# Kernel tuning notes

Hardware: AMD Instinct MI355X
Metric: run time of the kernel (lower is better)

## Reference

```python
import jax, jax.numpy as jnp
import numpy as np

B, L, D = 1, 2048, 768
H, DH = 12, 64  # n_heads, d_head (D // H)
LN_EPS = 1e-5
DEN_EPS = 1e-6


def setup_inputs() -> dict:
    key = jax.random.key(0)
    ks = jax.random.split(key, 11)
    s = 0.02
    return {
        "x": jax.random.normal(ks[0], (B, L, D), dtype=jnp.float32),
        "W_qkv": jax.random.normal(ks[1], (D, 3 * D), dtype=jnp.float32) * s,
        "b_qkv": jnp.zeros((3 * D,), dtype=jnp.float32),
        "W_sem": jax.random.normal(ks[2], (D, 2 * D), dtype=jnp.float32) * s,
        "b_sem": jnp.zeros((2 * D,), dtype=jnp.float32),
        "W_ctx": jax.random.normal(ks[3], (D, 2 * D), dtype=jnp.float32) * s,
        "b_ctx": jnp.zeros((2 * D,), dtype=jnp.float32),
        "W_proj": jax.random.normal(ks[4], (D, D), dtype=jnp.float32) * s,
        "b_proj": jnp.zeros((D,), dtype=jnp.float32),
        "ln_g": jnp.ones((D,), dtype=jnp.float32),
        "ln_b": jnp.zeros((D,), dtype=jnp.float32),
    }


def _heads(t):
    # [B,L,D] -> [B,H,L,DH]
    return t.reshape(B, L, H, DH).transpose(0, 2, 1, 3)


def reference(x, W_qkv, b_qkv, W_sem, b_sem, W_ctx, b_ctx, W_proj, b_proj, ln_g, ln_b):
    # LayerNorm
    mu = jnp.mean(x, axis=-1, keepdims=True)
    var = jnp.mean(jnp.square(x - mu), axis=-1, keepdims=True)
    x_norm = (x - mu) * jax.lax.rsqrt(var + LN_EPS) * ln_g + ln_b

    qkv = x_norm @ W_qkv + b_qkv
    q, k, v = jnp.split(qkv, 3, axis=-1)

    # interference gate from raw x
    sem = x @ W_sem + b_sem
    sem_amp = jax.nn.softplus(sem[..., :D])
    sem_phase = sem[..., D:]
    ctx = x @ W_ctx + b_ctx
    ctx_amp = jax.nn.softplus(ctx[..., :D])
    ctx_phase = ctx[..., D:]
    gate = jax.nn.sigmoid(sem_amp * ctx_amp * jnp.cos(sem_phase - ctx_phase))
    k = k * gate

    q_f = jax.nn.elu(_heads(q)) + 1.0  # [B,H,L,DH]
    k_f = jax.nn.elu(_heads(k)) + 1.0
    v_f = _heads(v)

    # causal linear attention: cumsum of kv outer products along L
    kv = jnp.einsum("bhld,bhle->bhlde", k_f, v_f)  # [B,H,L,DH,DH]
    kv_cum = jnp.cumsum(kv, axis=2)
    out_num = jnp.einsum("bhld,bhlde->bhle", q_f, kv_cum)  # [B,H,L,DH]

    k_cum = jnp.cumsum(k_f, axis=2)
    out_den = jnp.sum(q_f * k_cum, axis=-1, keepdims=True) + DEN_EPS

    attn = (out_num / out_den).transpose(0, 2, 1, 3).reshape(B, L, D)
    return attn @ W_proj + b_proj
```

## Files before the change

### kernel.cpp

```cpp
#include <hip/hip_runtime.h>
#include <math.h>

#define LSEQ 2048
#define DMODEL 768
#define NHEAD 12
#define DHEAD 64
#define NCHUNK 32
#define NMERGED 5376

typedef unsigned short ushort_t;
typedef __attribute__((ext_vector_type(8))) short short8;
typedef float float4v __attribute__((ext_vector_type(4)));

__device__ __forceinline__ ushort_t f2b(float f) {
    union { float f; unsigned int u; } v; v.f = f;
    unsigned int u = v.u;
    return (ushort_t)((u + 0x7fffu + ((u >> 16) & 1u)) >> 16);
}
__device__ __forceinline__ float b2f(ushort_t u) {
    union { unsigned int u; float f; } v; v.u = ((unsigned int)u) << 16;
    return v.f;
}

__device__ __forceinline__ void gl_lds16(const ushort_t* g, ushort_t* l) {
    __builtin_amdgcn_global_load_lds(
        (const __attribute__((address_space(1))) unsigned int*)g,
        (__attribute__((address_space(3))) unsigned int*)l, 16, 0, 0);
}

__global__ void ln_kernel(const float* __restrict__ x, const float* __restrict__ g,
                          const float* __restrict__ beta, ushort_t* __restrict__ xn,
                          ushort_t* __restrict__ xb) {
    int row = blockIdx.x;
    int tid = threadIdx.x;
    const float* xr = x + (size_t)row * DMODEL;
    float v0 = xr[tid], v1 = xr[tid + 256], v2 = xr[tid + 512];
    __shared__ float red[4];
    __shared__ float bc;
    float s = v0 + v1 + v2;
#pragma unroll
    for (int o = 32; o > 0; o >>= 1) s += __shfl_down(s, o);
    if ((tid & 63) == 0) red[tid >> 6] = s;
    __syncthreads();
    if (tid == 0) bc = (red[0] + red[1] + red[2] + red[3]) * (1.0f / DMODEL);
    __syncthreads();
    float mu = bc;
    float d0 = v0 - mu, d1 = v1 - mu, d2 = v2 - mu;
    float vs = d0 * d0 + d1 * d1 + d2 * d2;
    __syncthreads();
#pragma unroll
    for (int o = 32; o > 0; o >>= 1) vs += __shfl_down(vs, o);
    if ((tid & 63) == 0) red[tid >> 6] = vs;
    __syncthreads();
    if (tid == 0) bc = rsqrtf((red[0] + red[1] + red[2] + red[3]) * (1.0f / DMODEL) + 1e-5f);
    __syncthreads();
    float r = bc;
    ushort_t* xo = xn + (size_t)row * DMODEL;
    ushort_t* xc = xb + (size_t)row * DMODEL;
    xo[tid]       = f2b(d0 * r * g[tid]       + beta[tid]);
    xo[tid + 256] = f2b(d1 * r * g[tid + 256] + beta[tid + 256]);
    xo[tid + 512] = f2b(d2 * r * g[tid + 512] + beta[tid + 512]);
    xc[tid]       = f2b(v0);
    xc[tid + 256] = f2b(v1);
    xc[tid + 512] = f2b(v2);
}

__global__ void transpose_all_kernel(const float* __restrict__ Wq, const float* __restrict__ Ws,
                                     const float* __restrict__ Wc, ushort_t* __restrict__ Tm,
                                     const float* __restrict__ Wp, ushort_t* __restrict__ Tp) {
    const float* W; ushort_t* Wt; int N;
    switch (blockIdx.z) {
        case 0: W = Wq; Wt = Tm;                        N = 2304; break;
        case 1: W = Ws; Wt = Tm + (size_t)2304 * 768;   N = 1536; break;
        case 2: W = Wc; Wt = Tm + (size_t)3840 * 768;   N = 1536; break;
        default: W = Wp; Wt = Tp;                       N = 768;  break;
    }
    int nbase = blockIdx.x * 32;
    if (nbase >= N) return;
    __shared__ float tile[32][33];
    int tid = threadIdx.x;
    int tr = tid >> 5, tc = tid & 31;
    int kbase = blockIdx.y * 32;
#pragma unroll
    for (int p = 0; p < 4; p++) {
        int r = p * 8 + tr;
        tile[r][tc] = W[(size_t)(kbase + r) * N + nbase + tc];
    }
    __syncthreads();
#pragma unroll
    for (int p = 0; p < 4; p++) {
        int r = p * 8 + tr;
        Wt[(size_t)(nbase + r) * 768 + kbase + tc] = f2b(tile[tc][r]);
    }
}

__global__ __launch_bounds__(256) void gemm_merged_kernel(
    const ushort_t* __restrict__ Axn, const ushort_t* __restrict__ Axb,
    const ushort_t* __restrict__ Bt,
    const float* __restrict__ b_qkv, const float* __restrict__ b_sem,
    const float* __restrict__ b_ctx, float* __restrict__ C,
    ushort_t* __restrict__ vb) {
    const int K = 768, N = NMERGED;
    __shared__ ushort_t As[128 * 32];
    __shared__ ushort_t Bs[128 * 32];
    int tid = threadIdx.x;
    int wave = tid >> 6, lane = tid & 63;
    int wm = (wave >> 1) * 64, wn = (wave & 1) * 64;
    int quad = lane >> 4, l16 = lane & 15;
    int m0 = blockIdx.y * 128, n0 = blockIdx.x * 128;
    const ushort_t* A = (n0 < 2304) ? Axn : Axb;
    const float* bias = (n0 < 2304) ? (b_qkv + n0) : (n0 < 3840 ? (b_sem + n0 - 2304) : (b_ctx + n0 - 3840));

    int r0 = tid >> 2;
    int kc = (tid & 3) * 8;
    const ushort_t* Ag0 = A + (size_t)(m0 + r0) * K + kc;
    const ushort_t* Ag1 = A + (size_t)(m0 + 64 + r0) * K + kc;
    const ushort_t* Bg0 = Bt + (size_t)(n0 + r0) * K + kc;
    const ushort_t* Bg1 = Bt + (size_t)(n0 + 64 + r0) * K + kc;
    ushort_t* Al0 = &As[(wave * 64) * 8];
    ushort_t* Al1 = &As[(256 + wave * 64) * 8];
    ushort_t* Bl0 = &Bs[(wave * 64) * 8];
    ushort_t* Bl1 = &Bs[(256 + wave * 64) * 8];

    float4v acc[4][4];
#pragma unroll
    for (int i = 0; i < 4; i++)
#pragma unroll
        for (int j = 0; j < 4; j++)
#pragma unroll
            for (int r = 0; r < 4; r++) acc[i][j][r] = 0.0f;

    for (int k0 = 0; k0 < K; k0 += 32) {
        gl_lds16(Ag0 + k0, Al0);
        gl_lds16(Ag1 + k0, Al1);
        gl_lds16(Bg0 + k0, Bl0);
        gl_lds16(Bg1 + k0, Bl1);
        __syncthreads();
        short8 af[4], bf[4];
#pragma unroll
        for (int i = 0; i < 4; i++) af[i] = *(const short8*)&As[(wm + i * 16 + l16) * 32 + quad * 8];
#pragma unroll
        for (int j = 0; j < 4; j++) bf[j] = *(const short8*)&Bs[(wn + j * 16 + l16) * 32 + quad * 8];
#pragma unroll
        for (int i = 0; i < 4; i++)
#pragma unroll
            for (int j = 0; j < 4; j++)
                acc[i][j] = __builtin_amdgcn_mfma_f32_16x16x32_bf16(af[i], bf[j], acc[i][j], 0, 0, 0);
        __syncthreads();
    }
    bool is_v = (n0 >= 1536 && n0 < 2304);
#pragma unroll
    for (int i = 0; i < 4; i++) {
#pragma unroll
        for (int j = 0; j < 4; j++) {
            int colb = wn + j * 16 + l16;
            float bv = bias[colb];
#pragma unroll
            for (int r = 0; r < 4; r++) {
                int row = m0 + wm + i * 16 + quad * 4 + r;
                float o = acc[i][j][r] + bv;
                if (is_v) {
                    vb[(size_t)row * DMODEL + (n0 - 1536) + colb] = f2b(o);
                } else {
                    C[(size_t)row * N + n0 + colb] = o;
                }
            }
        }
    }
}

__global__ __launch_bounds__(256) void gemm_64_kernel(
    const ushort_t* __restrict__ A, const ushort_t* __restrict__ Bt,
    const float* __restrict__ bias, float* __restrict__ C,
    int N, int K) {
    __shared__ ushort_t As[64 * 32];
    __shared__ ushort_t Bs[64 * 32];
    int tid = threadIdx.x;
    int wave = tid >> 6, lane = tid & 63;
    int wm = (wave >> 1) * 32, wn = (wave & 1) * 32;
    int quad = lane >> 4, l16 = lane & 15;
    int m0 = blockIdx.y * 64, n0 = blockIdx.x * 64;

    int r0 = tid >> 2;
    int kc = (tid & 3) * 8;
    const ushort_t* Ag = A + (size_t)(m0 + r0) * K + kc;
    const ushort_t* Bg = Bt + (size_t)(n0 + r0) * K + kc;
    ushort_t* Al = &As[(wave * 16) * 32];
    ushort_t* Bl = &Bs[(wave * 16) * 32];

    float4v acc[2][2];
#pragma unroll
    for (int i = 0; i < 2; i++)
#pragma unroll
        for (int j = 0; j < 2; j++)
#pragma unroll
            for (int r = 0; r < 4; r++) acc[i][j][r] = 0.0f;

    for (int k0 = 0; k0 < K; k0 += 32) {
        gl_lds16(Ag + k0, Al);
        gl_lds16(Bg + k0, Bl);
        __syncthreads();
        short8 af[2], bf[2];
#pragma unroll
        for (int i = 0; i < 2; i++) af[i] = *(const short8*)&As[(wm + i * 16 + l16) * 32 + quad * 8];
#pragma unroll
        for (int j = 0; j < 2; j++) bf[j] = *(const short8*)&Bs[(wn + j * 16 + l16) * 32 + quad * 8];
#pragma unroll
        for (int i = 0; i < 2; i++)
#pragma unroll
            for (int j = 0; j < 2; j++)
                acc[i][j] = __builtin_amdgcn_mfma_f32_16x16x32_bf16(af[i], bf[j], acc[i][j], 0, 0, 0);
        __syncthreads();
    }
#pragma unroll
    for (int i = 0; i < 2; i++) {
#pragma unroll
        for (int j = 0; j < 2; j++) {
            int col = n0 + wn + j * 16 + l16;
            float bv = bias[col];
#pragma unroll
            for (int r = 0; r < 4; r++) {
                int row = m0 + wm + i * 16 + quad * 4 + r;
                C[(size_t)row * N + col] = acc[i][j][r] + bv;
            }
        }
    }
}

__device__ __forceinline__ float softplus_f(float x) {
    return (x > 15.f) ? x : log1pf(expf(x));
}

__global__ void gate_feat_kernel(const float* __restrict__ qsc,
                                 ushort_t* __restrict__ qf, ushort_t* __restrict__ kf) {
    int t = blockIdx.x * 256 + threadIdx.x;
    int l = t / 192, d = (t - l * 192) * 4;
    size_t base = (size_t)l * NMERGED;
    float sa[4], sp[4], ca[4], cp[4], q[4], k[4];
    *(float4*)sa = *(const float4*)&qsc[base + 2304 + d];
    *(float4*)sp = *(const float4*)&qsc[base + 3072 + d];
    *(float4*)ca = *(const float4*)&qsc[base + 3840 + d];
    *(float4*)cp = *(const float4*)&qsc[base + 4608 + d];
    *(float4*)q  = *(const float4*)&qsc[base + d];
    *(float4*)k  = *(const float4*)&qsc[base + 768 + d];
    ushort_t qo[4], ko[4];
#pragma unroll
    for (int j = 0; j < 4; j++) {
        float amp = softplus_f(sa[j]) * softplus_f(ca[j]);
        float tt = amp * cosf(sp[j] - cp[j]);
        float gate = 1.0f / (1.0f + expf(-tt));
        float kv = k[j] * gate;
        float qv = q[j];
        qo[j] = f2b((qv > 0.f) ? qv + 1.0f : expf(qv));
        ko[j] = f2b((kv > 0.f) ? kv + 1.0f : expf(kv));
    }
    size_t o = (size_t)l * DMODEL + d;
    *(uint2*)&qf[o] = *(uint2*)qo;
    *(uint2*)&kf[o] = *(uint2*)ko;
}

__global__ __launch_bounds__(256) void chunk_sum_mfma(const ushort_t* __restrict__ kf,
                                                      const ushort_t* __restrict__ vb,
                                                      float* __restrict__ S) {
    int h = blockIdx.x % NHEAD;
    int c = blockIdx.x / NHEAD;
    __shared__ ushort_t Kt[64 * 72];
    __shared__ ushort_t Vt[64 * 72];
    int tid = threadIdx.x;
    const size_t hb = (size_t)h * DHEAD;
#pragma unroll
    for (int it = 0; it < 4; it++) {
        int r = it * 16 + (tid >> 4);
        int cc = (tid & 15) * 4;
        int lg = c * 64 + r;
        ushort_t kt4[4], vt4[4];
        *(uint2*)kt4 = *(const uint2*)&kf[(size_t)lg * DMODEL + hb + cc];
        *(uint2*)vt4 = *(const uint2*)&vb[(size_t)lg * DMODEL + hb + cc];
#pragma unroll
        for (int i2 = 0; i2 < 4; i2++) {
            Kt[(cc + i2) * 72 + r] = kt4[i2];
            Vt[(cc + i2) * 72 + r] = vt4[i2];
        }
    }
    __syncthreads();
    int wave = tid >> 6, lane = tid & 63, quad = lane >> 4, l16 = lane & 15;
    int wm = wave * 16;
    float4v acc[4];
#pragma unroll
    for (int jt = 0; jt < 4; jt++)
#pragma unroll
        for (int r = 0; r < 4; r++) acc[jt][r] = 0.0f;
#pragma unroll
    for (int ks = 0; ks < 2; ks++) {
        short8 af = *(const short8*)&Kt[(wm + l16) * 72 + ks * 32 + quad * 8];
#pragma unroll
        for (int jt = 0; jt < 4; jt++) {
            short8 bf = *(const short8*)&Vt[(jt * 16 + l16) * 72 + ks * 32 + quad * 8];
            acc[jt] = __builtin_amdgcn_mfma_f32_16x16x32_bf16(af, bf, acc[jt], 0, 0, 0);
        }
    }
    float* Sp = S + (size_t)(h * NCHUNK + c) * 4160;
#pragma unroll
    for (int jt = 0; jt < 4; jt++) {
        float4 o;
        o.x = acc[jt][0]; o.y = acc[jt][1]; o.z = acc[jt][2]; o.w = acc[jt][3];
        *(float4*)&Sp[(jt * 16 + l16) * 64 + wm + quad * 4] = o;
    }
    if (tid < 64) {
        float s = 0.f;
#pragma unroll
        for (int g = 0; g < 8; g++) {
            short8 kv8 = *(const short8*)&Kt[tid * 72 + g * 8];
#pragma unroll
            for (int i2 = 0; i2 < 8; i2++) s += b2f(((ushort_t*)&kv8)[i2]);
        }
        Sp[4096 + tid] = s;
    }
}

__global__ void prefix_kernel(const float* __restrict__ S, ushort_t* __restrict__ Pb,
                              float* __restrict__ kpf) {
    int h = blockIdx.x;
    int i = blockIdx.y * 256 + threadIdx.x;
    if (i >= 4160) return;
    float v[NCHUNK];
    size_t base = (size_t)h * NCHUNK * 4160 + i;
#pragma unroll
    for (int c2 = 0; c2 < NCHUNK; c2++) v[c2] = S[base + (size_t)c2 * 4160];
    float run = 0.f;
    if (i < 4096) {
        size_t pb = (size_t)h * NCHUNK * 4096 + i;
#pragma unroll
        for (int c2 = 0; c2 < NCHUNK; c2++) {
            Pb[pb + (size_t)c2 * 4096] = f2b(run);
            run += v[c2];
        }
    } else {
        size_t kb = (size_t)h * NCHUNK * 64 + (i - 4096);
#pragma unroll
        for (int c2 = 0; c2 < NCHUNK; c2++) {
            kpf[kb + (size_t)c2 * 64] = run;
            run += v[c2];
        }
    }
}

__global__ __launch_bounds__(256) void attn_out_mfma(const ushort_t* __restrict__ qf,
                                                     const ushort_t* __restrict__ kf,
                                                     const ushort_t* __restrict__ vb,
                                                     const ushort_t* __restrict__ Pb,
                                                     const float* __restrict__ kpf,
                                                     ushort_t* __restrict__ attn) {
    int h = blockIdx.x % NHEAD;
    int c = blockIdx.x / NHEAD;
    __shared__ ushort_t Qs[64 * 72];
    __shared__ ushort_t Ks[64 * 72];
    __shared__ ushort_t Pt[64 * 72];
    __shared__ ushort_t Vt[64 * 72];
    __shared__ float Sc[64 * 68];
    __shared__ float kpl[64];
    __shared__ float denp[4][64];
    __shared__ float dnl[64];
    int tid = threadIdx.x;
    const size_t hb = (size_t)h * DHEAD;
    const size_t pcb = (size_t)(h * NCHUNK + c);
#pragma unroll
    for (int it = 0; it < 2; it++) {
        int chunk = it * 256 + tid;
        int r = chunk >> 3, c8 = (chunk & 7) * 8;
        int lg = c * 64 + r;
        *(uint4*)&Qs[r * 72 + c8] = *(const uint4*)&qf[(size_t)lg * DMODEL + hb + c8];
        *(uint4*)&Ks[r * 72 + c8] = *(const uint4*)&kf[(size_t)lg * DMODEL + hb + c8];
        *(uint4*)&Pt[r * 72 + c8] = *(const uint4*)&Pb[pcb * 4096 + r * 64 + c8];
    }
#pragma unroll
    for (int it = 0; it < 4; it++) {
        int r = it * 16 + (tid >> 4);
        int cc = (tid & 15) * 4;
        int lg = c * 64 + r;
        ushort_t vt4[4];
        *(uint2*)vt4 = *(const uint2*)&vb[(size_t)lg * DMODEL + hb + cc];
#pragma unroll
        for (int i2 = 0; i2 < 4; i2++) Vt[(cc + i2) * 72 + r] = vt4[i2];
    }
    if (tid < 64) kpl[tid] = kpf[pcb * 64 + tid];
    __syncthreads();
    int wave = tid >> 6, lane = tid & 63, quad = lane >> 4, l16 = lane & 15;
    int wm = wave * 16;
    float4v s_acc[4], n_acc[4];
#pragma unroll
    for (int jt = 0; jt < 4; jt++)
#pragma unroll
        for (int r = 0; r < 4; r++) { s_acc[jt][r] = 0.0f; n_acc[jt][r] = 0.0f; }
#pragma unroll
    for (int ks = 0; ks < 2; ks++) {
        short8 aq = *(const short8*)&Qs[(wm + l16) * 72 + ks * 32 + quad * 8];
#pragma unroll
        for (int jt = 0; jt < 4; jt++) {
            short8 bk = *(const short8*)&Ks[(jt * 16 + l16) * 72 + ks * 32 + quad * 8];
            short8 bp = *(const short8*)&Pt[(jt * 16 + l16) * 72 + ks * 32 + quad * 8];
            s_acc[jt] = __builtin_amdgcn_mfma_f32_16x16x32_bf16(aq, bk, s_acc[jt], 0, 0, 0);
            n_acc[jt] = __builtin_amdgcn_mfma_f32_16x16x32_bf16(aq, bp, n_acc[jt], 0, 0, 0);
        }
    }
#pragma unroll
    for (int jt = 0; jt < 4; jt++)
#pragma unroll
        for (int r = 0; r < 4; r++)
            Sc[(wm + quad * 4 + r) * 68 + jt * 16 + l16] = s_acc[jt][r];
    __syncthreads();
    {
        int l = tid & 63, part = tid >> 6;
        float s = 0.f;
#pragma unroll
        for (int jj = 0; jj < 16; jj++) {
            int j = part * 16 + jj;
            float v = Sc[l * 68 + j];
            s += (j <= l) ? v : 0.f;
        }
#pragma unroll
        for (int dd = 0; dd < 16; dd++) {
            int d = part * 16 + dd;
            s += b2f(Qs[l * 72 + d]) * kpl[d];
        }
        denp[part][l] = s;
    }
    __syncthreads();
    if (tid < 64) dnl[tid] = denp[0][tid] + denp[1][tid] + denp[2][tid] + denp[3][tid] + 1e-6f;
    __syncthreads();
#pragma unroll
    for (int ks = 0; ks < 2; ks++) {
        int m = wm + l16;
        float sv[8];
        *(float4*)&sv[0] = *(const float4*)&Sc[m * 68 + ks * 32 + quad * 8];
        *(float4*)&sv[4] = *(const float4*)&Sc[m * 68 + ks * 32 + quad * 8 + 4];
        ushort_t am[8];
#pragma unroll
        for (int i2 = 0; i2 < 8; i2++) {
            int j = ks * 32 + quad * 8 + i2;
            am[i2] = (j <= m) ? f2b(sv[i2]) : (ushort_t)0;
        }
        short8 af = *(short8*)am;
#pragma unroll
        for (int jt = 0; jt < 4; jt++) {
            short8 bv = *(const short8*)&Vt[(jt * 16 + l16) * 72 + ks * 32 + quad * 8];
            n_acc[jt] = __builtin_amdgcn_mfma_f32_16x16x32_bf16(af, bv, n_acc[jt], 0, 0, 0);
        }
    }
#pragma unroll
    for (int jt = 0; jt < 4; jt++) {
        int e = jt * 16 + l16;
#pragma unroll
        for (int r = 0; r < 4; r++) {
            int l = wm + quad * 4 + r;
            float o = n_acc[jt][r] / dnl[l];
            attn[(size_t)(c * 64 + l) * DMODEL + hb + e] = f2b(o);
        }
    }
}

extern "C" void kernel_launch(void* const* d_in, const int* in_sizes, int n_in,
                              void* d_out, int out_size, void* d_ws, size_t ws_size,
                              hipStream_t stream) {
    const float* x      = (const float*)d_in[0];
    const float* W_qkv  = (const float*)d_in[1];
    const float* b_qkv  = (const float*)d_in[2];
    const float* W_sem  = (const float*)d_in[3];
    const float* b_sem  = (const float*)d_in[4];
    const float* W_ctx  = (const float*)d_in[5];
    const float* b_ctx  = (const float*)d_in[6];
    const float* W_proj = (const float*)d_in[7];
    const float* b_proj = (const float*)d_in[8];
    const float* ln_g   = (const float*)d_in[9];
    const float* ln_b   = (const float*)d_in[10];
    float* out = (float*)d_out;
    float* ws  = (float*)d_ws;

    ushort_t* Wt_merged = (ushort_t*)(ws);
    ushort_t* Wt_proj   = (ushort_t*)(ws + 2064384);
    ushort_t* xb        = (ushort_t*)(ws + 2359296);
    ushort_t* xnb       = (ushort_t*)(ws + 3145728);
    float*    qsc       = ws + 3932160;
    ushort_t* vb        = (ushort_t*)(ws + 14942208);
    ushort_t* qf        = (ushort_t*)(ws + 2359296);
    ushort_t* kf        = (ushort_t*)(ws + 3145728);
    float*    S         = ws;
    ushort_t* Pb        = (ushort_t*)(ws + 3932160);
    float*    kpf       = ws + 4718592;
    ushort_t* attnb     = (ushort_t*)(ws);

    ln_kernel<<<LSEQ, 256, 0, stream>>>(x, ln_g, ln_b, xnb, xb);
    transpose_all_kernel<<<dim3(72, 24, 4), 256, 0, stream>>>(W_qkv, W_sem, W_ctx, Wt_merged,
                                                              W_proj, Wt_proj);

    gemm_merged_kernel<<<dim3(NMERGED / 128, LSEQ / 128), 256, 0, stream>>>(
        xnb, xb, Wt_merged, b_qkv, b_sem, b_ctx, qsc, vb);

    gate_feat_kernel<<<(LSEQ * DMODEL / 4) / 256, 256, 0, stream>>>(qsc, qf, kf);
    chunk_sum_mfma<<<NHEAD * NCHUNK, 256, 0, stream>>>(kf, vb, S);
    prefix_kernel<<<dim3(NHEAD, 17), 256, 0, stream>>>(S, Pb, kpf);
    attn_out_mfma<<<NHEAD * NCHUNK, 256, 0, stream>>>(qf, kf, vb, Pb, kpf, attnb);

    gemm_64_kernel<<<dim3(768 / 64, LSEQ / 64), 256, 0, stream>>>(attnb, Wt_proj, b_proj, out, 768, 768);
}
```

Before: 163.4 us.

## Fuse LN with weight transpose, gate into chunk-sum, store GEMM outputs as bf16

Merges the layernorm and weight-transpose kernels into one launch, and fuses the gating/feature-map computation into the chunk-sum MFMA kernel, which removes two launches. The merged GEMM now writes bf16 instead of fp32, halving intermediate traffic. It also remaps block IDs so each XCD gets a contiguous tile range, aiming for better L2 locality. The bf16 rounding of the pre-activation gate inputs before softplus/cos adds numerical error.

```diff
diff --git a/kernel.cpp b/kernel.cpp
--- a/kernel.cpp
+++ b/kernel.cpp
@@ -28,69 +28,73 @@
         (__attribute__((address_space(3))) unsigned int*)l, 16, 0, 0);
 }
 
-__global__ void ln_kernel(const float* __restrict__ x, const float* __restrict__ g,
-                          const float* __restrict__ beta, ushort_t* __restrict__ xn,
-                          ushort_t* __restrict__ xb) {
-    int row = blockIdx.x;
-    int tid = threadIdx.x;
-    const float* xr = x + (size_t)row * DMODEL;
-    float v0 = xr[tid], v1 = xr[tid + 256], v2 = xr[tid + 512];
+__global__ void pre_kernel(const float* __restrict__ x, const float* __restrict__ g,
+                           const float* __restrict__ beta, ushort_t* __restrict__ xn,
+                           ushort_t* __restrict__ xb,
+                           const float* __restrict__ Wq, const float* __restrict__ Ws,
+                           const float* __restrict__ Wc, ushort_t* __restrict__ Tm,
+                           const float* __restrict__ Wp, ushort_t* __restrict__ Tp) {
     __shared__ float red[4];
     __shared__ float bc;
-    float s = v0 + v1 + v2;
-#pragma unroll
-    for (int o = 32; o > 0; o >>= 1) s += __shfl_down(s, o);
-    if ((tid & 63) == 0) red[tid >> 6] = s;
-    __syncthreads();
-    if (tid == 0) bc = (red[0] + red[1] + red[2] + red[3]) * (1.0f / DMODEL);
-    __syncthreads();
-    float mu = bc;
-    float d0 = v0 - mu, d1 = v1 - mu, d2 = v2 - mu;
-    float vs = d0 * d0 + d1 * d1 + d2 * d2;
-    __syncthreads();
-#pragma unroll
-    for (int o = 32; o > 0; o >>= 1) vs += __shfl_down(vs, o);
-    if ((tid & 63) == 0) red[tid >> 6] = vs;
-    __syncthreads();
-    if (tid == 0) bc = rsqrtf((red[0] + red[1] + red[2] + red[3]) * (1.0f / DMODEL) + 1e-5f);
-    __syncthreads();
-    float r = bc;
-    ushort_t* xo = xn + (size_t)row * DMODEL;
-    ushort_t* xc = xb + (size_t)row * DMODEL;
-    xo[tid]       = f2b(d0 * r * g[tid]       + beta[tid]);
-    xo[tid + 256] = f2b(d1 * r * g[tid + 256] + beta[tid + 256]);
-    xo[tid + 512] = f2b(d2 * r * g[tid + 512] + beta[tid + 512]);
-    xc[tid]       = f2b(v0);
-    xc[tid + 256] = f2b(v1);
-    xc[tid + 512] = f2b(v2);
-}
-
-__global__ void transpose_all_kernel(const float* __restrict__ Wq, const float* __restrict__ Ws,
-                                     const float* __restrict__ Wc, ushort_t* __restrict__ Tm,
-                                     const float* __restrict__ Wp, ushort_t* __restrict__ Tp) {
-    const float* W; ushort_t* Wt; int N;
-    switch (blockIdx.z) {
-        case 0: W = Wq; Wt = Tm;                        N = 2304; break;
-        case 1: W = Ws; Wt = Tm + (size_t)2304 * 768;   N = 1536; break;
-        case 2: W = Wc; Wt = Tm + (size_t)3840 * 768;   N = 1536; break;
-        default: W = Wp; Wt = Tp;                       N = 768;  break;
-    }
-    int nbase = blockIdx.x * 32;
-    if (nbase >= N) return;
     __shared__ float tile[32][33];
     int tid = threadIdx.x;
-    int tr = tid >> 5, tc = tid & 31;
-    int kbase = blockIdx.y * 32;
-#pragma unroll
-    for (int p = 0; p < 4; p++) {
-        int r = p * 8 + tr;
-        tile[r][tc] = W[(size_t)(kbase + r) * N + nbase + tc];
-    }
-    __syncthreads();
-#pragma unroll
-    for (int p = 0; p < 4; p++) {
-        int r = p * 8 + tr;
-        Wt[(size_t)(nbase + r) * 768 + kbase + tc] = f2b(tile[tc][r]);
+    if (blockIdx.x < 2048) {
+        int row = blockIdx.x;
+        const float* xr = x + (size_t)row * DMODEL;
+        float v0 = xr[tid], v1 = xr[tid + 256], v2 = xr[tid + 512];
+        float s = v0 + v1 + v2;
+#pragma unroll
+        for (int o = 32; o > 0; o >>= 1) s += __shfl_down(s, o);
+        if ((tid & 63) == 0) red[tid >> 6] = s;
+        __syncthreads();
+        if (tid == 0) bc = (red[0] + red[1] + red[2] + red[3]) * (1.0f / DMODEL);
+        __syncthreads();
+        float mu = bc;
+        float d0 = v0 - mu, d1 = v1 - mu, d2 = v2 - mu;
+        float vs = d0 * d0 + d1 * d1 + d2 * d2;
+        __syncthreads();
+#pragma unroll
+        for (int o = 32; o > 0; o >>= 1) vs += __shfl_down(vs, o);
+        if ((tid & 63) == 0) red[tid >> 6] = vs;
+        __syncthreads();
+        if (tid == 0) bc = rsqrtf((red[0] + red[1] + red[2] + red[3]) * (1.0f / DMODEL) + 1e-5f);
+        __syncthreads();
+        float r = bc;
+        ushort_t* xo = xn + (size_t)row * DMODEL;
+        ushort_t* xc = xb + (size_t)row * DMODEL;
+        xo[tid]       = f2b(d0 * r * g[tid]       + beta[tid]);
+        xo[tid + 256] = f2b(d1 * r * g[tid + 256] + beta[tid + 256]);
+        xo[tid + 512] = f2b(d2 * r * g[tid + 512] + beta[tid + 512]);
+        xc[tid]       = f2b(v0);
+        xc[tid + 256] = f2b(v1);
+        xc[tid + 512] = f2b(v2);
+    } else {
+        int bid = blockIdx.x - 2048;
+        int nb = bid % 72;
+        int kb = (bid / 72) % 24;
+        int zb = bid / (72 * 24);
+        const float* W; ushort_t* Wt; int N;
+        switch (zb) {
+            case 0: W = Wq; Wt = Tm;                        N = 2304; break;
+            case 1: W = Ws; Wt = Tm + (size_t)2304 * 768;   N = 1536; break;
+            case 2: W = Wc; Wt = Tm + (size_t)3840 * 768;   N = 1536; break;
+            default: W = Wp; Wt = Tp;                       N = 768;  break;
+        }
+        int nbase = nb * 32;
+        if (nbase >= N) return;
+        int tr = tid >> 5, tc = tid & 31;
+        int kbase = kb * 32;
+#pragma unroll
+        for (int p = 0; p < 4; p++) {
+            int r = p * 8 + tr;
+            tile[r][tc] = W[(size_t)(kbase + r) * N + nbase + tc];
+        }
+        __syncthreads();
+#pragma unroll
+        for (int p = 0; p < 4; p++) {
+            int r = p * 8 + tr;
+            Wt[(size_t)(nbase + r) * 768 + kbase + tc] = f2b(tile[tc][r]);
+        }
     }
 }
 
@@ -98,16 +102,20 @@
     const ushort_t* __restrict__ Axn, const ushort_t* __restrict__ Axb,
     const ushort_t* __restrict__ Bt,
     const float* __restrict__ b_qkv, const float* __restrict__ b_sem,
-    const float* __restrict__ b_ctx, float* __restrict__ C,
+    const float* __restrict__ b_ctx, ushort_t* __restrict__ Cb,
     ushort_t* __restrict__ vb) {
-    const int K = 768, N = NMERGED;
+    const int K = 768;
     __shared__ ushort_t As[128 * 32];
     __shared__ ushort_t Bs[128 * 32];
     int tid = threadIdx.x;
     int wave = tid >> 6, lane = tid & 63;
     int wm = (wave >> 1) * 64, wn = (wave & 1) * 64;
     int quad = lane >> 4, l16 = lane & 15;
-    int m0 = blockIdx.y * 128, n0 = blockIdx.x * 128;
+    int bid = blockIdx.x;
+    int xcd = bid & 7, slot = bid >> 3;
+    int tile_id = xcd * 84 + slot;
+    int m0 = (tile_id & 15) * 128;
+    int n0 = (tile_id >> 4) * 128;
     const ushort_t* A = (n0 < 2304) ? Axn : Axb;
     const float* bias = (n0 < 2304) ? (b_qkv + n0) : (n0 < 3840 ? (b_sem + n0 - 2304) : (b_ctx + n0 - 3840));
 
@@ -158,11 +166,11 @@
 #pragma unroll
             for (int r = 0; r < 4; r++) {
                 int row = m0 + wm + i * 16 + quad * 4 + r;
-                float o = acc[i][j][r] + bv;
+                ushort_t o = f2b(acc[i][j][r] + bv);
                 if (is_v) {
-                    vb[(size_t)row * DMODEL + (n0 - 1536) + colb] = f2b(o);
+                    vb[(size_t)row * DMODEL + (n0 - 1536) + colb] = o;
                 } else {
-                    C[(size_t)row * N + n0 + colb] = o;
+                    Cb[(size_t)row * NMERGED + n0 + colb] = o;
                 }
             }
         }
@@ -231,56 +239,47 @@
     return (x > 15.f) ? x : log1pf(expf(x));
 }
 
-__global__ void gate_feat_kernel(const float* __restrict__ qsc,
-                                 ushort_t* __restrict__ qf, ushort_t* __restrict__ kf) {
-    int t = blockIdx.x * 256 + threadIdx.x;
-    int l = t / 192, d = (t - l * 192) * 4;
-    size_t base = (size_t)l * NMERGED;
-    float sa[4], sp[4], ca[4], cp[4], q[4], k[4];
-    *(float4*)sa = *(const float4*)&qsc[base + 2304 + d];
-    *(float4*)sp = *(const float4*)&qsc[base + 3072 + d];
-    *(float4*)ca = *(const float4*)&qsc[base + 3840 + d];
-    *(float4*)cp = *(const float4*)&qsc[base + 4608 + d];
-    *(float4*)q  = *(const float4*)&qsc[base + d];
-    *(float4*)k  = *(const float4*)&qsc[base + 768 + d];
-    ushort_t qo[4], ko[4];
-#pragma unroll
-    for (int j = 0; j < 4; j++) {
-        float amp = softplus_f(sa[j]) * softplus_f(ca[j]);
-        float tt = amp * cosf(sp[j] - cp[j]);
-        float gate = 1.0f / (1.0f + expf(-tt));
-        float kv = k[j] * gate;
-        float qv = q[j];
-        qo[j] = f2b((qv > 0.f) ? qv + 1.0f : expf(qv));
-        ko[j] = f2b((kv > 0.f) ? kv + 1.0f : expf(kv));
-    }
-    size_t o = (size_t)l * DMODEL + d;
-    *(uint2*)&qf[o] = *(uint2*)qo;
-    *(uint2*)&kf[o] = *(uint2*)ko;
-}
-
-__global__ __launch_bounds__(256) void chunk_sum_mfma(const ushort_t* __restrict__ kf,
-                                                      const ushort_t* __restrict__ vb,
-                                                      float* __restrict__ S) {
+__global__ __launch_bounds__(256) void chunk_gate_mfma(const ushort_t* __restrict__ qscb,
+                                                       const ushort_t* __restrict__ vb,
+                                                       ushort_t* __restrict__ qf,
+                                                       ushort_t* __restrict__ kf,
+                                                       float* __restrict__ S) {
     int h = blockIdx.x % NHEAD;
     int c = blockIdx.x / NHEAD;
     __shared__ ushort_t Kt[64 * 72];
     __shared__ ushort_t Vt[64 * 72];
     int tid = threadIdx.x;
-    const size_t hb = (size_t)h * DHEAD;
+    const int hb = h * DHEAD;
 #pragma unroll
     for (int it = 0; it < 4; it++) {
         int r = it * 16 + (tid >> 4);
         int cc = (tid & 15) * 4;
         int lg = c * 64 + r;
-        ushort_t kt4[4], vt4[4];
-        *(uint2*)kt4 = *(const uint2*)&kf[(size_t)lg * DMODEL + hb + cc];
+        size_t qb = (size_t)lg * NMERGED + hb + cc;
+        ushort_t q4[4], k4[4], sa4[4], sp4[4], ca4[4], cp4[4], vt4[4];
+        *(uint2*)q4  = *(const uint2*)&qscb[qb];
+        *(uint2*)k4  = *(const uint2*)&qscb[qb + 768];
+        *(uint2*)sa4 = *(const uint2*)&qscb[qb + 2304];
+        *(uint2*)sp4 = *(const uint2*)&qscb[qb + 3072];
+        *(uint2*)ca4 = *(const uint2*)&qscb[qb + 3840];
+        *(uint2*)cp4 = *(const uint2*)&qscb[qb + 4608];
         *(uint2*)vt4 = *(const uint2*)&vb[(size_t)lg * DMODEL + hb + cc];
+        ushort_t qo[4], ko[4];
 #pragma unroll
         for (int i2 = 0; i2 < 4; i2++) {
-            Kt[(cc + i2) * 72 + r] = kt4[i2];
+            float amp = softplus_f(b2f(sa4[i2])) * softplus_f(b2f(ca4[i2]));
+            float tt = amp * cosf(b2f(sp4[i2]) - b2f(cp4[i2]));
+            float gate = 1.0f / (1.0f + expf(-tt));
+            float kv = b2f(k4[i2]) * gate;
+            float qv = b2f(q4[i2]);
+            qo[i2] = f2b((qv > 0.f) ? qv + 1.0f : expf(qv));
+            ko[i2] = f2b((kv > 0.f) ? kv + 1.0f : expf(kv));
+            Kt[(cc + i2) * 72 + r] = ko[i2];
             Vt[(cc + i2) * 72 + r] = vt4[i2];
         }
+        size_t o = (size_t)lg * DMODEL + hb + cc;
+        *(uint2*)&qf[o] = *(uint2*)qo;
+        *(uint2*)&kf[o] = *(uint2*)ko;
     }
     __syncthreads();
     int wave = tid >> 6, lane = tid & 63, quad = lane >> 4, l16 = lane & 15;
@@ -480,7 +479,7 @@
     ushort_t* Wt_proj   = (ushort_t*)(ws + 2064384);
     ushort_t* xb        = (ushort_t*)(ws + 2359296);
     ushort_t* xnb       = (ushort_t*)(ws + 3145728);
-    float*    qsc       = ws + 3932160;
+    ushort_t* qscb      = (ushort_t*)(ws + 3932160);
     ushort_t* vb        = (ushort_t*)(ws + 14942208);
     ushort_t* qf        = (ushort_t*)(ws + 2359296);
     ushort_t* kf        = (ushort_t*)(ws + 3145728);
@@ -489,15 +488,14 @@
     float*    kpf       = ws + 4718592;
     ushort_t* attnb     = (ushort_t*)(ws);
 
-    ln_kernel<<<LSEQ, 256, 0, stream>>>(x, ln_g, ln_b, xnb, xb);
-    transpose_all_kernel<<<dim3(72, 24, 4), 256, 0, stream>>>(W_qkv, W_sem, W_ctx, Wt_merged,
-                                                              W_proj, Wt_proj);
-
-    gemm_merged_kernel<<<dim3(NMERGED / 128, LSEQ / 128), 256, 0, stream>>>(
-        xnb, xb, Wt_merged, b_qkv, b_sem, b_ctx, qsc, vb);
-
-    gate_feat_kernel<<<(LSEQ * DMODEL / 4) / 256, 256, 0, stream>>>(qsc, qf, kf);
-    chunk_sum_mfma<<<NHEAD * NCHUNK, 256, 0, stream>>>(kf, vb, S);
+    pre_kernel<<<2048 + 72 * 24 * 4, 256, 0, stream>>>(x, ln_g, ln_b, xnb, xb,
+                                                       W_qkv, W_sem, W_ctx, Wt_merged,
+                                                       W_proj, Wt_proj);
+
+    gemm_merged_kernel<<<672, 256, 0, stream>>>(
+        xnb, xb, Wt_merged, b_qkv, b_sem, b_ctx, qscb, vb);
+
+    chunk_gate_mfma<<<NHEAD * NCHUNK, 256, 0, stream>>>(qscb, vb, qf, kf, S);
     prefix_kernel<<<dim3(NHEAD, 17), 256, 0, stream>>>(S, Pb, kpf);
     attn_out_mfma<<<NHEAD * NCHUNK, 256, 0, stream>>>(qf, kf, vb, Pb, kpf, attnb);
 
```

New measurement: 165.7 us. Within noise of the previous version (+1.4%).
